# Kernel optimization log

Measured on AMD Instinct MI355X. Metric: run time of the kernel, lower is better.

Reference implementation:

```python
import jax, jax.numpy as jnp
import numpy as np

EMB = 1024
HEADS = 16
HEAD_DIM = EMB // HEADS
EPS = 1e-5


def layer_norm(x, scale, shift):
    mean = jnp.mean(x, axis=-1, keepdims=True)
    var = jnp.mean(jnp.square(x - mean), axis=-1, keepdims=True)  # unbiased=False
    return scale * ((x - mean) / jnp.sqrt(var + EPS)) + shift


def gelu_tanh(x):
    c = jnp.sqrt(jnp.asarray(2.0 / jnp.pi, x.dtype))
    return 0.5 * x * (1.0 + jnp.tanh(c * (x + 0.044715 * x * x * x)))


def setup_inputs() -> dict:
    key = jax.random.key(0)
    ks = jax.random.split(key, 12)
    s = 0.02
    B, S, D = 2, 2048, EMB
    return {
        "x": jax.random.normal(ks[0], (B, S, D), jnp.float32),
        "wq": jax.random.normal(ks[1], (D, D), jnp.float32) * s,
        "wk": jax.random.normal(ks[2], (D, D), jnp.float32) * s,
        "wv": jax.random.normal(ks[3], (D, D), jnp.float32) * s,
        "wo": jax.random.normal(ks[4], (D, D), jnp.float32) * s,
        "bo": jnp.zeros((D,), jnp.float32),
        "w1": jax.random.normal(ks[5], (D, 4 * D), jnp.float32) * s,
        "b1": jnp.zeros((4 * D,), jnp.float32),
        "w2": jax.random.normal(ks[6], (4 * D, D), jnp.float32) * s,
        "b2": jnp.zeros((D,), jnp.float32),
        "g1": jnp.ones((D,), jnp.float32),
        "s1": jnp.zeros((D,), jnp.float32),
        "g2": jnp.ones((D,), jnp.float32),
        "s2": jnp.zeros((D,), jnp.float32),
    }


def reference(x, wq, wk, wv, wo, bo, w1, b1, w2, b2, g1, s1, g2, s2):
    B, S, D = x.shape
    # --- attention sub-block ---
    h = layer_norm(x, g1, s1)
    q = (h @ wq).reshape(B, S, HEADS, HEAD_DIM).transpose(0, 2, 1, 3)  # [B,H,S,d]
    k = (h @ wk).reshape(B, S, HEADS, HEAD_DIM).transpose(0, 2, 1, 3)
    v = (h @ wv).reshape(B, S, HEADS, HEAD_DIM).transpose(0, 2, 1, 3)
    scores = jnp.einsum("bhqd,bhkd->bhqk", q, k)
    causal = jnp.tril(jnp.ones((S, S), bool))  # True = keep
    scores = jnp.where(causal, scores, -jnp.inf)
    attn = jax.nn.softmax(scores / jnp.sqrt(jnp.asarray(HEAD_DIM, x.dtype)), axis=-1)
    ctx = jnp.einsum("bhqk,bhkd->bhqd", attn, v).transpose(0, 2, 1, 3).reshape(B, S, D)
    x = x + (ctx @ wo + bo)
    # --- FFN sub-block ---
    h = layer_norm(x, g2, s2)
    h = gelu_tanh(h @ w1 + b1) @ w2 + b2
    return x + h
```

## Files before the change

kernel.cpp:

```cpp
#include <hip/hip_runtime.h>


typedef __attribute__((ext_vector_type(8))) short s16x8;
typedef __attribute__((ext_vector_type(4))) float f32x4;
typedef __attribute__((ext_vector_type(16))) float f32x16;
typedef unsigned short u16;
typedef unsigned int u32;

#define DEV static __device__ __forceinline__
#define MFMA16 __builtin_amdgcn_mfma_f32_16x16x32_bf16
#define MFMA32 __builtin_amdgcn_mfma_f32_32x32x16_bf16
#define GLOAD_LDS16(gp, lp)                                         \
  __builtin_amdgcn_global_load_lds(                                 \
      (const __attribute__((address_space(1))) void*)(gp),          \
      (__attribute__((address_space(3))) void*)(lp), 16, 0, 0)

DEV u16 f2bf(float f) {
  union { float f; unsigned u; } c; c.f = f;
  unsigned u = c.u;
  u += 0x7fff + ((u >> 16) & 1);
  return (u16)(u >> 16);
}

DEV u32 cvtpk(float lo, float hi) {
  u32 r;
  asm("v_cvt_pk_bf16_f32 %0, %1, %2" : "=v"(r) : "v"(lo), "v"(hi));
  return r;
}

DEV float gelu_tanh(float v) {
  const float c0 = 0.7978845608028654f;
  float u = c0 * (v + 0.044715f * v * v * v);
  return 0.5f * v * (1.0f + tanhf(u));
}

DEV s16x8 ld8(const u16* p) { return *(const s16x8*)p; }

__global__ __launch_bounds__(256) void tconv_kernel(
    const float* __restrict__ W, u16* __restrict__ Wt, int K, int N) {
  __shared__ u16 T[64][80];
  const int t = threadIdx.x;
  const int n0 = blockIdx.x * 64, k0 = blockIdx.y * 64;
  const int kr = t >> 4, nc = (t & 15) * 4;
#pragma unroll
  for (int p = 0; p < 4; ++p) {
    const int k = p * 16 + kr;
    float4 v = *(const float4*)(W + (size_t)(k0 + k) * N + n0 + nc);
    T[nc + 0][k] = f2bf(v.x);
    T[nc + 1][k] = f2bf(v.y);
    T[nc + 2][k] = f2bf(v.z);
    T[nc + 3][k] = f2bf(v.w);
  }
  __syncthreads();
  const int nr = t >> 2, kc = (t & 3) * 16;
  *(s16x8*)(Wt + (size_t)(n0 + nr) * K + k0 + kc) = *(const s16x8*)&T[nr][kc];
  *(s16x8*)(Wt + (size_t)(n0 + nr) * K + k0 + kc + 8) =
      *(const s16x8*)&T[nr][kc + 8];
}

__global__ __launch_bounds__(256) void ln_kernel(
    const float* __restrict__ x, const float* __restrict__ g,
    const float* __restrict__ b, u16* __restrict__ out) {
  const int row = blockIdx.x;
  const int t = threadIdx.x;
  const float* xr = x + (size_t)row * 1024;
  float4 v = *(const float4*)(xr + t * 4);
  float s = v.x + v.y + v.z + v.w;
  float ss = v.x * v.x + v.y * v.y + v.z * v.z + v.w * v.w;
#pragma unroll
  for (int off = 1; off < 64; off <<= 1) {
    s += __shfl_xor(s, off);
    ss += __shfl_xor(ss, off);
  }
  __shared__ float sb[4], ssb[4];
  const int w = t >> 6;
  if ((t & 63) == 0) { sb[w] = s; ssb[w] = ss; }
  __syncthreads();
  s = sb[0] + sb[1] + sb[2] + sb[3];
  ss = ssb[0] + ssb[1] + ssb[2] + ssb[3];
  const float mean = s * (1.0f / 1024.0f);
  const float var = ss * (1.0f / 1024.0f) - mean * mean;
  const float rstd = rsqrtf(var + 1e-5f);
  const int c = t * 4;
  ushort4 o;
  o.x = f2bf(g[c + 0] * ((v.x - mean) * rstd) + b[c + 0]);
  o.y = f2bf(g[c + 1] * ((v.y - mean) * rstd) + b[c + 1]);
  o.z = f2bf(g[c + 2] * ((v.z - mean) * rstd) + b[c + 2]);
  o.w = f2bf(g[c + 3] * ((v.w - mean) * rstd) + b[c + 3]);
  *(ushort4*)(out + (size_t)row * 1024 + c) = o;
}

DEV void gemm_stage(const u16* __restrict__ A, const u16* __restrict__ Bt,
                    int bm, int bn, int K, int kof, u16 (*Al)[32],
                    u16 (*Bl)[32], int w, int lane) {
  const int srow = lane >> 2;
  const int scol = ((lane & 3) ^ ((lane >> 3) & 3)) * 8;
#pragma unroll
  for (int p = 0; p < 2; ++p) {
    const int r0 = (w * 2 + p) * 16;
    GLOAD_LDS16(A + (size_t)(bm + r0 + srow) * K + kof + scol, &Al[r0][0]);
    GLOAD_LDS16(Bt + (size_t)(bn + r0 + srow) * K + kof + scol, &Bl[r0][0]);
  }
}

DEV void gemm_step(const u16 (*Al)[32], const u16 (*Bl)[32],
                   f32x4 (&acc)[4][4], int wm, int wn, int lr, int lg) {
  const int cs = (lg ^ ((lr >> 1) & 3)) * 8;
  s16x8 af[4], bf[4];
#pragma unroll
  for (int i = 0; i < 4; ++i) {
    af[i] = *(const s16x8*)&Al[wm + i * 16 + lr][cs];
    bf[i] = *(const s16x8*)&Bl[wn + i * 16 + lr][cs];
  }
#pragma unroll
  for (int i = 0; i < 4; ++i)
#pragma unroll
    for (int j = 0; j < 4; ++j)
      acc[i][j] = MFMA16(af[i], bf[j], acc[i][j], 0, 0, 0);
}

template <int EPI>
__global__ __launch_bounds__(256) void gemm_kernel(
    const u16* __restrict__ A, const u16* __restrict__ Bt,
    const float* __restrict__ bias, const float* __restrict__ res,
    void* __restrict__ Cv, int M, int N, int K) {
  __shared__ __align__(16) u16 Al[2][128][32];
  __shared__ __align__(16) u16 Bl[2][128][32];
  const int t = threadIdx.x;
  const int lane = t & 63, w = t >> 6;
  const int wm = (w >> 1) * 64, wn = (w & 1) * 64;
  int bid = blockIdx.y * gridDim.x + blockIdx.x;
  const int q8 = (gridDim.x * gridDim.y) >> 3;
  bid = (bid & 7) * q8 + (bid >> 3);
  const int bm = (bid / gridDim.x) * 128, bn = (bid % gridDim.x) * 128;
  const int lr = lane & 15, lg = lane >> 4;
  f32x4 acc[4][4] = {};
  const int nkt = K >> 5;

  gemm_stage(A, Bt, bm, bn, K, 0, Al[0], Bl[0], w, lane);
  __syncthreads();
  for (int kt = 0; kt < nkt - 1; ++kt) {
    const int cur = kt & 1;
    gemm_stage(A, Bt, bm, bn, K, (kt + 1) << 5, Al[cur ^ 1], Bl[cur ^ 1], w,
               lane);
    gemm_step(Al[cur], Bl[cur], acc, wm, wn, lr, lg);
    __syncthreads();
  }
  gemm_step(Al[(nkt - 1) & 1], Bl[(nkt - 1) & 1], acc, wm, wn, lr, lg);

#pragma unroll
  for (int i = 0; i < 4; ++i) {
    const int row = bm + wm + i * 16 + lg * 4;
#pragma unroll
    for (int j = 0; j < 4; ++j) {
      const int col = bn + wn + j * 16 + lr;
      if (EPI == 0) {
        const int bb = row >> 11, sloc = row & 2047;
        const int which = col >> 10, n = col & 1023;
        const int hh = n >> 6, dd = n & 63;
        u16* qbuf = (u16*)Cv;
        if (which == 2) {
          ushort4 o;
          o.x = f2bf(acc[i][j][0]); o.y = f2bf(acc[i][j][1]);
          o.z = f2bf(acc[i][j][2]); o.w = f2bf(acc[i][j][3]);
          *(ushort4*)(qbuf + 8388608 +
                      (size_t)((bb * 16 + hh) * 64 + dd) * 2048 + sloc) = o;
        } else {
          const float sc = (which == 0) ? 0.18033688011112042f : 1.0f;
          u16* dst = qbuf + (size_t)which * 4194304 +
                     ((size_t)(bb * 16 + hh) * 2048 + sloc) * 64 + dd;
#pragma unroll
          for (int e = 0; e < 4; ++e) dst[(size_t)e * 64] = f2bf(acc[i][j][e] * sc);
        }
      } else if (EPI == 1) {
        float* C = (float*)Cv;
        const float bs = bias[col];
#pragma unroll
        for (int e = 0; e < 4; ++e)
          C[(size_t)(row + e) * N + col] =
              acc[i][j][e] + bs + res[(size_t)(row + e) * N + col];
      } else {
        u16* C = (u16*)Cv;
        const float bs = bias[col];
#pragma unroll
        for (int e = 0; e < 4; ++e)
          C[(size_t)(row + e) * N + col] = f2bf(gelu_tanh(acc[i][j][e] + bs));
      }
    }
  }
}

DEV void g64_stage(const u16* __restrict__ A, const u16* __restrict__ Bt,
                   int bm, int bn, int K, int kof, u16 (*Al)[32],
                   u16 (*Bl)[32], int w, int lane) {
  const int srow = lane >> 2;
  const int scol = ((lane & 3) ^ ((lane >> 3) & 3)) * 8;
  const int r0 = w << 4;
  GLOAD_LDS16(A + (size_t)(bm + r0 + srow) * K + kof + scol, &Al[r0][0]);
  GLOAD_LDS16(Bt + (size_t)(bn + r0 + srow) * K + kof + scol, &Bl[r0][0]);
}

DEV void g64_step(const u16 (*Al)[32], const u16 (*Bl)[32],
                  f32x4 (&acc)[2][2], int wm, int wn, int lr, int lg) {
  const int cs = (lg ^ ((lr >> 1) & 3)) * 8;
  s16x8 af[2], bf[2];
#pragma unroll
  for (int i = 0; i < 2; ++i) {
    af[i] = *(const s16x8*)&Al[wm + i * 16 + lr][cs];
    bf[i] = *(const s16x8*)&Bl[wn + i * 16 + lr][cs];
  }
#pragma unroll
  for (int i = 0; i < 2; ++i)
#pragma unroll
    for (int j = 0; j < 2; ++j)
      acc[i][j] = MFMA16(af[i], bf[j], acc[i][j], 0, 0, 0);
}

template <int EPI>
__global__ __launch_bounds__(256) void gemm64_kernel(
    const u16* __restrict__ A, const u16* __restrict__ Bt,
    const float* __restrict__ bias, const float* __restrict__ res,
    void* __restrict__ Cv, int M, int N, int K) {
  __shared__ __align__(16) u16 Al[2][64][32];
  __shared__ __align__(16) u16 Bl[2][64][32];
  const int t = threadIdx.x;
  const int lane = t & 63, w = t >> 6;
  const int wm = (w >> 1) * 32, wn = (w & 1) * 32;
  int bid = blockIdx.y * gridDim.x + blockIdx.x;
  const int q8 = (gridDim.x * gridDim.y) >> 3;
  bid = (bid & 7) * q8 + (bid >> 3);
  const int bm = (bid / gridDim.x) * 64, bn = (bid % gridDim.x) * 64;
  const int lr = lane & 15, lg = lane >> 4;
  f32x4 acc[2][2] = {};
  const int nkt = K >> 5;

  g64_stage(A, Bt, bm, bn, K, 0, Al[0], Bl[0], w, lane);
  __syncthreads();
  for (int kt = 0; kt < nkt - 1; ++kt) {
    const int cur = kt & 1;
    g64_stage(A, Bt, bm, bn, K, (kt + 1) << 5, Al[cur ^ 1], Bl[cur ^ 1], w,
              lane);
    g64_step(Al[cur], Bl[cur], acc, wm, wn, lr, lg);
    __syncthreads();
  }
  g64_step(Al[(nkt - 1) & 1], Bl[(nkt - 1) & 1], acc, wm, wn, lr, lg);

#pragma unroll
  for (int i = 0; i < 2; ++i) {
    const int row = bm + wm + i * 16 + lg * 4;
#pragma unroll
    for (int j = 0; j < 2; ++j) {
      const int col = bn + wn + j * 16 + lr;
      if (EPI == 1) {
        float* C = (float*)Cv;
        const float bs = bias[col];
#pragma unroll
        for (int e = 0; e < 4; ++e)
          C[(size_t)(row + e) * N + col] =
              acc[i][j][e] + bs + res[(size_t)(row + e) * N + col];
      } else {
        u16* C = (u16*)Cv;
        const float bs = bias[col];
#pragma unroll
        for (int e = 0; e < 4; ++e)
          C[(size_t)(row + e) * N + col] = f2bf(gelu_tanh(acc[i][j][e] + bs));
      }
    }
  }
}

DEV void g256_stage(const u16* __restrict__ A, const u16* __restrict__ Bt,
                    int bm, int bn, int K, int kof, u16 (*Al)[32],
                    u16 (*Bl)[32], int w, int lane) {
  const int srow = lane >> 2;
  const int scol = ((lane & 3) ^ ((lane >> 3) & 3)) * 8;
#pragma unroll
  for (int c = 0; c < 2; ++c) {
    const int r0 = (w << 5) + (c << 4);
    GLOAD_LDS16(A + (size_t)(bm + r0 + srow) * K + kof + scol, &Al[r0][0]);
    GLOAD_LDS16(Bt + (size_t)(bn + r0 + srow) * K + kof + scol, &Bl[r0][0]);
  }
}

DEV void g256_step(const u16 (*Al)[32], const u16 (*Bl)[32],
                   f32x4 (&acc)[8][4], int wm, int wn, int lr, int lg) {
  const int cs = (lg ^ ((lr >> 1) & 3)) * 8;
  s16x8 af[8], bf[4];
#pragma unroll
  for (int i = 0; i < 8; ++i)
    af[i] = *(const s16x8*)&Al[wm + i * 16 + lr][cs];
#pragma unroll
  for (int j = 0; j < 4; ++j)
    bf[j] = *(const s16x8*)&Bl[wn + j * 16 + lr][cs];
#pragma unroll
  for (int i = 0; i < 8; ++i)
#pragma unroll
    for (int j = 0; j < 4; ++j)
      acc[i][j] = MFMA16(af[i], bf[j], acc[i][j], 0, 0, 0);
}

template <int EPI>
__global__ __launch_bounds__(512, 2) void gemm256_kernel(
    const u16* __restrict__ A, const u16* __restrict__ Bt,
    const float* __restrict__ bias, const float* __restrict__ res,
    void* __restrict__ Cv, int M, int N, int K) {
  __shared__ __align__(16) u16 Al[2][256][32];
  __shared__ __align__(16) u16 Bl[2][256][32];
  const int t = threadIdx.x;
  const int lane = t & 63, w = t >> 6;
  const int wm = (w >> 2) << 7;
  const int wn = (w & 3) << 6;
  int bid = blockIdx.y * gridDim.x + blockIdx.x;
  const int q8 = (gridDim.x * gridDim.y) >> 3;
  bid = (bid & 7) * q8 + (bid >> 3);
  const int bm = (bid / gridDim.x) << 8, bn = (bid % gridDim.x) << 8;
  const int lr = lane & 15, lg = lane >> 4;
  f32x4 acc[8][4] = {};
  const int nkt = K >> 5;

  g256_stage(A, Bt, bm, bn, K, 0, Al[0], Bl[0], w, lane);
  __syncthreads();
  for (int kt = 0; kt < nkt - 1; ++kt) {
    const int cur = kt & 1;
    g256_stage(A, Bt, bm, bn, K, (kt + 1) << 5, Al[cur ^ 1], Bl[cur ^ 1], w,
               lane);
    g256_step(Al[cur], Bl[cur], acc, wm, wn, lr, lg);
    __syncthreads();
  }
  g256_step(Al[(nkt - 1) & 1], Bl[(nkt - 1) & 1], acc, wm, wn, lr, lg);

#pragma unroll
  for (int i = 0; i < 8; ++i) {
    const int row = bm + wm + i * 16 + lg * 4;
#pragma unroll
    for (int j = 0; j < 4; ++j) {
      const int col = bn + wn + j * 16 + lr;
      if (EPI == 1) {
        float* C = (float*)Cv;
        const float bs = bias[col];
#pragma unroll
        for (int e = 0; e < 4; ++e)
          C[(size_t)(row + e) * N + col] =
              acc[i][j][e] + bs + res[(size_t)(row + e) * N + col];
      } else {
        u16* C = (u16*)Cv;
        const float bs = bias[col];
#pragma unroll
        for (int e = 0; e < 4; ++e)
          C[(size_t)(row + e) * N + col] = f2bf(gelu_tanh(acc[i][j][e] + bs));
      }
    }
  }
}

DEV float vmax16(const f32x16& v) {
  float a = fmaxf(v[0], v[1]), b = fmaxf(v[2], v[3]);
  float c = fmaxf(v[4], v[5]), d = fmaxf(v[6], v[7]);
  float e = fmaxf(v[8], v[9]), f = fmaxf(v[10], v[11]);
  float g = fmaxf(v[12], v[13]), h = fmaxf(v[14], v[15]);
  a = fmaxf(a, b); c = fmaxf(c, d); e = fmaxf(e, f); g = fmaxf(g, h);
  return fmaxf(fmaxf(a, c), fmaxf(e, g));
}
DEV float vsum16(const f32x16& v) {
  float a = v[0] + v[1], b = v[2] + v[3];
  float c = v[4] + v[5], d = v[6] + v[7];
  float e = v[8] + v[9], f = v[10] + v[11];
  float g = v[12] + v[13], h = v[14] + v[15];
  a += b; c += d; e += f; g += h;
  return (a + c) + (e + g);
}

struct A32 {
  s16x8 q[4];
  f32x16 o0, o1;
  float m, l;
};

template <int MODE>
DEV void body32(A32& st, int k0, const u16* Kb, const u16* Vb, int la,
                int hi) {
  s16x8 ka0[4], ka1[4];
#pragma unroll
  for (int c = 0; c < 4; ++c)
    ka0[c] = ld8(Kb + (size_t)(k0 + la) * 64 + c * 16 + hi * 8);
  if (MODE != 2)
#pragma unroll
    for (int c = 0; c < 4; ++c)
      ka1[c] = ld8(Kb + (size_t)(k0 + 32 + la) * 64 + c * 16 + hi * 8);
  f32x16 s0, s1;
#pragma unroll
  for (int r = 0; r < 16; ++r) { s0[r] = 0.f; s1[r] = 0.f; }
#pragma unroll
  for (int c = 0; c < 4; ++c) s0 = MFMA32(ka0[c], st.q[c], s0, 0, 0, 0);
  if (MODE != 2)
#pragma unroll
    for (int c = 0; c < 4; ++c) s1 = MFMA32(ka1[c], st.q[c], s1, 0, 0, 0);
  const int nkc = (MODE == 2) ? 2 : 4;
  s16x8 va0[4], va1[4];
#pragma unroll
  for (int kc = 0; kc < 4; ++kc)
    if (kc < nkc) {
      va0[kc] = ld8(Vb + (size_t)la * 2048 + k0 + kc * 16 + hi * 8);
      va1[kc] = ld8(Vb + (size_t)(32 + la) * 2048 + k0 + kc * 16 + hi * 8);
    }
  if (MODE == 1) {
#pragma unroll
    for (int r = 0; r < 16; ++r) {
      const int kl = (r & 3) + 8 * (r >> 2) + 4 * hi;
      if (kl > la) s1[r] = -INFINITY;
    }
  }
  if (MODE == 2) {
#pragma unroll
    for (int r = 0; r < 16; ++r) {
      const int kl = (r & 3) + 8 * (r >> 2) + 4 * hi;
      if (kl > la) s0[r] = -INFINITY;
    }
  }
  float mt = vmax16(s0);
  if (MODE != 2) mt = fmaxf(mt, vmax16(s1));
  mt = fmaxf(mt, __shfl_xor(mt, 32));
  const float mn = fmaxf(st.m, mt);
  const float sf = exp2f(st.m - mn);
#pragma unroll
  for (int r = 0; r < 16; ++r) s0[r] = exp2f(s0[r] - mn);
  if (MODE != 2)
#pragma unroll
    for (int r = 0; r < 16; ++r) s1[r] = exp2f(s1[r] - mn);
  float rs = vsum16(s0);
  if (MODE != 2) rs += vsum16(s1);
  rs += __shfl_xor(rs, 32);
  st.l = st.l * sf + rs;
  st.m = mn;
#pragma unroll
  for (int r = 0; r < 16; ++r) { st.o0[r] *= sf; st.o1[r] *= sf; }
  const int nh = (MODE == 2) ? 1 : 2;
#pragma unroll
  for (int half = 0; half < nh; ++half) {
    u32 w[8];
#pragma unroll
    for (int i = 0; i < 8; ++i)
      w[i] = half ? cvtpk(s1[2 * i], s1[2 * i + 1])
                  : cvtpk(s0[2 * i], s0[2 * i + 1]);
#pragma unroll
    for (int kp = 0; kp < 2; ++kp) {
      const u32 w0 = w[4 * kp + 0], w1 = w[4 * kp + 1];
      const u32 w2 = w[4 * kp + 2], w3 = w[4 * kp + 3];
      const u32 t0 = hi ? w0 : w2, t1 = hi ? w1 : w3;
      const u32 x0 = (u32)__shfl_xor((int)t0, 32);
      const u32 x1 = (u32)__shfl_xor((int)t1, 32);
      union { u32 u[4]; s16x8 v; } bb;
      bb.u[0] = hi ? x0 : w0;
      bb.u[1] = hi ? x1 : w1;
      bb.u[2] = hi ? w2 : x0;
      bb.u[3] = hi ? w3 : x1;
      const int kc = half * 2 + kp;
      st.o0 = MFMA32(va0[kc], bb.v, st.o0, 0, 0, 0);
      st.o1 = MFMA32(va1[kc], bb.v, st.o1, 0, 0, 0);
    }
  }
}

DEV void a32_init(A32& st, const u16* Qbase, int qs, int la, int hi) {
#pragma unroll
  for (int c = 0; c < 4; ++c)
    st.q[c] = ld8(Qbase + (size_t)(qs + la) * 64 + c * 16 + hi * 8);
#pragma unroll
  for (int r = 0; r < 16; ++r) { st.o0[r] = 0.f; st.o1[r] = 0.f; }
  st.m = -INFINITY;
  st.l = 0.f;
}

DEV void a32_fin(const A32& st, u16* __restrict__ ctx, int bh, int qs, int la,
                 int hi) {
  const int bb = bh >> 4, hh = bh & 15;
  const float inv = 1.0f / st.l;
  u16* crow = ctx + (size_t)(bb * 2048 + qs + la) * 1024 + hh * 64;
#pragma unroll
  for (int r = 0; r < 16; r += 2) {
    const int d = (r & 3) + 8 * (r >> 2) + 4 * hi;
    *(u32*)(crow + d) = cvtpk(st.o0[r] * inv, st.o0[r + 1] * inv);
    *(u32*)(crow + 32 + d) = cvtpk(st.o1[r] * inv, st.o1[r + 1] * inv);
  }
}

template <bool ODD>
DEV void chain_tail(A32& st, int nfull, int qs, const u16* Kb, const u16* Vb,
                    int la, int hi) {
  if (ODD) body32<1>(st, nfull * 64, Kb, Vb, la, hi);
  else     body32<2>(st, qs, Kb, Vb, la, hi);
}

__global__ __launch_bounds__(64) void attn_kernel(
    const u16* __restrict__ Qg, const u16* __restrict__ Kg,
    const u16* __restrict__ Vt, u16* __restrict__ ctx) {
  const int lane = threadIdx.x & 63;
  const int la = lane & 31, hi = lane >> 5;
  const int tA = blockIdx.x;
  const int bh = blockIdx.y;
  const int tB = 63 - tA;
  const int qsA = tA * 32, qsB = tB * 32;
  const int nfA = tA >> 1, nfB = tB >> 1;
  const size_t baseK = (size_t)bh * 2048 * 64;
  const size_t baseV = (size_t)bh * 64 * 2048;
  const u16* Kb = Kg + baseK;
  const u16* Vb = Vt + baseV;

  A32 A, B;
  a32_init(A, Qg + baseK, qsA, la, hi);
  a32_init(B, Qg + baseK, qsB, la, hi);

  for (int kt = 0; kt < nfA; ++kt) {
    body32<0>(B, kt * 64, Kb, Vb, la, hi);
    body32<0>(A, kt * 64, Kb, Vb, la, hi);
  }
  body32<0>(B, nfA * 64, Kb, Vb, la, hi);
  if (tA & 1) chain_tail<true>(A, nfA, qsA, Kb, Vb, la, hi);
  else        chain_tail<false>(A, nfA, qsA, Kb, Vb, la, hi);
  a32_fin(A, ctx, bh, qsA, la, hi);

  for (int kt = nfA + 1; kt < nfB; ++kt)
    body32<0>(B, kt * 64, Kb, Vb, la, hi);
  if (tB & 1) chain_tail<true>(B, nfB, qsB, Kb, Vb, la, hi);
  else        chain_tail<false>(B, nfB, qsB, Kb, Vb, la, hi);
  a32_fin(B, ctx, bh, qsB, la, hi);
}

extern "C" void kernel_launch(void* const* d_in, const int* in_sizes, int n_in,
                              void* d_out, int out_size, void* d_ws,
                              size_t ws_size, hipStream_t stream) {
  const float* x  = (const float*)d_in[0];
  const float* wq = (const float*)d_in[1];
  const float* wk = (const float*)d_in[2];
  const float* wv = (const float*)d_in[3];
  const float* wo = (const float*)d_in[4];
  const float* bo = (const float*)d_in[5];
  const float* w1 = (const float*)d_in[6];
  const float* b1 = (const float*)d_in[7];
  const float* w2 = (const float*)d_in[8];
  const float* b2 = (const float*)d_in[9];
  const float* g1 = (const float*)d_in[10];
  const float* s1 = (const float*)d_in[11];
  const float* g2 = (const float*)d_in[12];
  const float* s2 = (const float*)d_in[13];
  float* out = (float*)d_out;

  const size_t MB = (size_t)1 << 20;
  char* p = (char*)d_ws;
  u16* hb    = (u16*)(p + 0 * MB);
  u16* qbuf  = (u16*)(p + 8 * MB);
  u16* ctxb  = (u16*)(p + 32 * MB);
  float* x2  = (float*)(p + 40 * MB);
  u16* h2b   = (u16*)(p + 56 * MB);
  u16* qkvw  = (u16*)(p + 64 * MB);
  u16* wot   = (u16*)(p + 70 * MB);
  u16* w1t   = (u16*)(p + 72 * MB);
  u16* w2t   = (u16*)(p + 80 * MB);
  u16* gb    = (u16*)(p + 0 * MB);

  const dim3 blk(256);
  tconv_kernel<<<dim3(16, 16), blk, 0, stream>>>(wq, qkvw, 1024, 1024);
  tconv_kernel<<<dim3(16, 16), blk, 0, stream>>>(wk, qkvw + 1048576, 1024, 1024);
  tconv_kernel<<<dim3(16, 16), blk, 0, stream>>>(wv, qkvw + 2097152, 1024, 1024);
  tconv_kernel<<<dim3(16, 16), blk, 0, stream>>>(wo, wot, 1024, 1024);
  tconv_kernel<<<dim3(64, 16), blk, 0, stream>>>(w1, w1t, 1024, 4096);
  tconv_kernel<<<dim3(16, 64), blk, 0, stream>>>(w2, w2t, 4096, 1024);

  ln_kernel<<<4096, blk, 0, stream>>>(x, g1, s1, hb);
  gemm_kernel<0><<<dim3(24, 32), blk, 0, stream>>>(hb, qkvw, nullptr, nullptr,
                                                   qbuf, 4096, 3072, 1024);
  attn_kernel<<<dim3(32, 32), dim3(64), 0, stream>>>(
      qbuf, qbuf + 4194304, qbuf + 8388608, ctxb);
  gemm64_kernel<1><<<dim3(16, 64), blk, 0, stream>>>(ctxb, wot, bo, x, x2,
                                                     4096, 1024, 1024);
  ln_kernel<<<4096, blk, 0, stream>>>(x2, g2, s2, h2b);
  gemm256_kernel<2><<<dim3(16, 16), dim3(512), 0, stream>>>(
      h2b, w1t, b1, nullptr, gb, 4096, 4096, 1024);
  gemm64_kernel<1><<<dim3(16, 64), blk, 0, stream>>>(gb, w2t, b2, x2, out,
                                                     4096, 1024, 4096);
}
```

Measured before the change: 302.5 us.

## Split attention KV range across two blocks with combine pass, merge weight conversions

Result: no change. 301.6 us (-0.3%).

```diff
diff --git a/kernel.cpp b/kernel.cpp
--- a/kernel.cpp
+++ b/kernel.cpp
@@ -22,6 +22,11 @@
   return (u16)(u >> 16);
 }
 
+DEV float bf2f(u16 v) {
+  union { u32 u; float f; } c; c.u = (u32)v << 16;
+  return c.f;
+}
+
 DEV u32 cvtpk(float lo, float hi) {
   u32 r;
   asm("v_cvt_pk_bf16_f32 %0, %1, %2" : "=v"(r) : "v"(lo), "v"(hi));
@@ -36,11 +41,10 @@
 
 DEV s16x8 ld8(const u16* p) { return *(const s16x8*)p; }
 
-__global__ __launch_bounds__(256) void tconv_kernel(
-    const float* __restrict__ W, u16* __restrict__ Wt, int K, int N) {
+DEV void tconv_tile(const float* __restrict__ W, u16* __restrict__ Wt, int K,
+                    int N, int bx, int by, int t) {
   __shared__ u16 T[64][80];
-  const int t = threadIdx.x;
-  const int n0 = blockIdx.x * 64, k0 = blockIdx.y * 64;
+  const int n0 = bx * 64, k0 = by * 64;
   const int kr = t >> 4, nc = (t & 15) * 4;
 #pragma unroll
   for (int p = 0; p < 4; ++p) {
@@ -56,6 +60,29 @@
   *(s16x8*)(Wt + (size_t)(n0 + nr) * K + k0 + kc) = *(const s16x8*)&T[nr][kc];
   *(s16x8*)(Wt + (size_t)(n0 + nr) * K + k0 + kc + 8) =
       *(const s16x8*)&T[nr][kc + 8];
+}
+
+__global__ __launch_bounds__(256) void tconv_all(
+    const float* __restrict__ wq, const float* __restrict__ wk,
+    const float* __restrict__ wv, const float* __restrict__ wo,
+    const float* __restrict__ w1, const float* __restrict__ w2,
+    u16* __restrict__ qkvw, u16* __restrict__ wot, u16* __restrict__ w1t,
+    u16* __restrict__ w2t) {
+  const int idx = blockIdx.x, t = threadIdx.x;
+  if (idx < 768) {
+    const int which = idx >> 8, r = idx & 255;
+    const float* W = which == 0 ? wq : (which == 1 ? wk : wv);
+    tconv_tile(W, qkvw + which * 1048576, 1024, 1024, r & 15, r >> 4, t);
+  } else if (idx < 1024) {
+    const int r = idx - 768;
+    tconv_tile(wo, wot, 1024, 1024, r & 15, r >> 4, t);
+  } else if (idx < 2048) {
+    const int r = idx - 1024;
+    tconv_tile(w1, w1t, 1024, 4096, r & 63, r >> 6, t);
+  } else {
+    const int r = idx - 2048;
+    tconv_tile(w2, w2t, 4096, 1024, r & 15, r >> 4, t);
+  }
 }
 
 __global__ __launch_bounds__(256) void ln_kernel(
@@ -420,8 +447,9 @@
   float mt = vmax16(s0);
   if (MODE != 2) mt = fmaxf(mt, vmax16(s1));
   mt = fmaxf(mt, __shfl_xor(mt, 32));
-  const float mn = fmaxf(st.m, mt);
-  const float sf = exp2f(st.m - mn);
+  const bool skip = __all(mt <= st.m + 8.0f) != 0;
+  const float mn = skip ? st.m : fmaxf(st.m, mt);
+  const float sf = skip ? 1.0f : exp2f(st.m - mn);
 #pragma unroll
   for (int r = 0; r < 16; ++r) s0[r] = exp2f(s0[r] - mn);
   if (MODE != 2)
@@ -430,10 +458,12 @@
   float rs = vsum16(s0);
   if (MODE != 2) rs += vsum16(s1);
   rs += __shfl_xor(rs, 32);
-  st.l = st.l * sf + rs;
+  st.l = skip ? (st.l + rs) : (st.l * sf + rs);
   st.m = mn;
-#pragma unroll
-  for (int r = 0; r < 16; ++r) { st.o0[r] *= sf; st.o1[r] *= sf; }
+  if (!skip) {
+#pragma unroll
+    for (int r = 0; r < 16; ++r) { st.o0[r] *= sf; st.o1[r] *= sf; }
+  }
   const int nh = (MODE == 2) ? 1 : 2;
 #pragma unroll
   for (int half = 0; half < nh; ++half) {
@@ -471,36 +501,45 @@
   st.l = 0.f;
 }
 
-DEV void a32_fin(const A32& st, u16* __restrict__ ctx, int bh, int qs, int la,
-                 int hi) {
-  const int bb = bh >> 4, hh = bh & 15;
-  const float inv = 1.0f / st.l;
-  u16* crow = ctx + (size_t)(bb * 2048 + qs + la) * 1024 + hh * 64;
+DEV void a32_emit(const A32& st, u16* __restrict__ pO, float* __restrict__ pml,
+                  int p, int la, int hi) {
+  u16* po = pO + (size_t)p * 2048 + la * 64;
 #pragma unroll
   for (int r = 0; r < 16; r += 2) {
     const int d = (r & 3) + 8 * (r >> 2) + 4 * hi;
-    *(u32*)(crow + d) = cvtpk(st.o0[r] * inv, st.o0[r + 1] * inv);
-    *(u32*)(crow + 32 + d) = cvtpk(st.o1[r] * inv, st.o1[r + 1] * inv);
-  }
-}
-
-template <bool ODD>
-DEV void chain_tail(A32& st, int nfull, int qs, const u16* Kb, const u16* Vb,
-                    int la, int hi) {
-  if (ODD) body32<1>(st, nfull * 64, Kb, Vb, la, hi);
-  else     body32<2>(st, qs, Kb, Vb, la, hi);
+    *(u32*)(po + d) = cvtpk(st.o0[r], st.o0[r + 1]);
+    *(u32*)(po + 32 + d) = cvtpk(st.o1[r], st.o1[r + 1]);
+  }
+  if (hi == 0) {
+    pml[p * 64 + la] = st.m;
+    pml[p * 64 + 32 + la] = st.l;
+  }
+}
+
+DEV void body_tail(A32& st, int t, const u16* Kb, const u16* Vb, int la,
+                   int hi) {
+  const int nf = t >> 1;
+  if (t & 1) body32<1>(st, nf * 64, Kb, Vb, la, hi);
+  else       body32<2>(st, nf * 64, Kb, Vb, la, hi);
 }
 
 __global__ __launch_bounds__(64) void attn_kernel(
     const u16* __restrict__ Qg, const u16* __restrict__ Kg,
-    const u16* __restrict__ Vt, u16* __restrict__ ctx) {
+    const u16* __restrict__ Vt, u16* __restrict__ pO,
+    float* __restrict__ pml) {
   const int lane = threadIdx.x & 63;
   const int la = lane & 31, hi = lane >> 5;
-  const int tA = blockIdx.x;
+  const int tA = blockIdx.x >> 1, h = blockIdx.x & 1;
   const int bh = blockIdx.y;
   const int tB = 63 - tA;
   const int qsA = tA * 32, qsB = tB * 32;
-  const int nfA = tA >> 1, nfB = tB >> 1;
+  const int nA = (tA >> 1) + 1, nB = (tB >> 1) + 1;
+  const int cA = (nA + 1) >> 1, cB = (nB + 1) >> 1;
+  const int a0 = h ? cA : 0, a1 = h ? nA : cA;
+  const int b0 = h ? cB : 0, b1 = h ? nB : cB;
+  const int aiEnd = min(a1, nA - 1), biEnd = min(b1, nB - 1);
+  const bool aTail = (a1 == nA) && (a1 > a0);
+  const bool bTail = (b1 == nB) && (b1 > b0);
   const size_t baseK = (size_t)bh * 2048 * 64;
   const size_t baseV = (size_t)bh * 64 * 2048;
   const u16* Kb = Kg + baseK;
@@ -510,20 +549,54 @@
   a32_init(A, Qg + baseK, qsA, la, hi);
   a32_init(B, Qg + baseK, qsB, la, hi);
 
-  for (int kt = 0; kt < nfA; ++kt) {
-    body32<0>(B, kt * 64, Kb, Vb, la, hi);
-    body32<0>(A, kt * 64, Kb, Vb, la, hi);
-  }
-  body32<0>(B, nfA * 64, Kb, Vb, la, hi);
-  if (tA & 1) chain_tail<true>(A, nfA, qsA, Kb, Vb, la, hi);
-  else        chain_tail<false>(A, nfA, qsA, Kb, Vb, la, hi);
-  a32_fin(A, ctx, bh, qsA, la, hi);
-
-  for (int kt = nfA + 1; kt < nfB; ++kt)
-    body32<0>(B, kt * 64, Kb, Vb, la, hi);
-  if (tB & 1) chain_tail<true>(B, nfB, qsB, Kb, Vb, la, hi);
-  else        chain_tail<false>(B, nfB, qsB, Kb, Vb, la, hi);
-  a32_fin(B, ctx, bh, qsB, la, hi);
+  int ia = a0, ib = b0;
+  const int common = min(aiEnd - a0, biEnd - b0);
+  for (int i = 0; i < common; ++i) {
+    body32<0>(B, ib * 64, Kb, Vb, la, hi); ++ib;
+    body32<0>(A, ia * 64, Kb, Vb, la, hi); ++ia;
+  }
+  for (; ib < biEnd; ++ib) body32<0>(B, ib * 64, Kb, Vb, la, hi);
+  for (; ia < aiEnd; ++ia) body32<0>(A, ia * 64, Kb, Vb, la, hi);
+  if (bTail) body_tail(B, tB, Kb, Vb, la, hi);
+  if (aTail) body_tail(A, tA, Kb, Vb, la, hi);
+
+  const int pA = (((bh << 6) | tA) << 1) | h;
+  const int pB = (((bh << 6) | tB) << 1) | h;
+  a32_emit(A, pO, pml, pA, la, hi);
+  a32_emit(B, pO, pml, pB, la, hi);
+}
+
+__global__ __launch_bounds__(64) void attn_combine(
+    const u16* __restrict__ pO, const float* __restrict__ pml,
+    u16* __restrict__ ctx) {
+  const int t = blockIdx.x, bh = blockIdx.y;
+  const int lane = threadIdx.x & 63;
+  const int la = lane & 31, hi = lane >> 5;
+  const int p0 = ((bh << 6) | t) << 1;
+  const float m0 = pml[p0 * 64 + la], l0 = pml[p0 * 64 + 32 + la];
+  const float m1 = pml[(p0 + 1) * 64 + la], l1 = pml[(p0 + 1) * 64 + 32 + la];
+  const float M = fmaxf(m0, m1);
+  const float w0 = exp2f(m0 - M), w1 = exp2f(m1 - M);
+  const float inv = 1.0f / (l0 * w0 + l1 * w1);
+  const float f0 = w0 * inv, f1 = w1 * inv;
+  const u16* o0 = pO + (size_t)p0 * 2048 + la * 64 + hi * 32;
+  const u16* o1 = o0 + 2048;
+  const int bb = bh >> 4, hh = bh & 15;
+  u16* crow = ctx + (size_t)(bb * 2048 + t * 32 + la) * 1024 + hh * 64 +
+              hi * 32;
+#pragma unroll
+  for (int j = 0; j < 32; j += 8) {
+    s16x8 a = ld8(o0 + j), b = ld8(o1 + j);
+    union { u32 u[4]; s16x8 v; } o;
+#pragma unroll
+    for (int i = 0; i < 4; ++i) {
+      const float e0 = bf2f((u16)a[2 * i]) * f0 + bf2f((u16)b[2 * i]) * f1;
+      const float e1 =
+          bf2f((u16)a[2 * i + 1]) * f0 + bf2f((u16)b[2 * i + 1]) * f1;
+      o.u[i] = cvtpk(e0, e1);
+    }
+    *(s16x8*)(crow + j) = o.v;
+  }
 }
 
 extern "C" void kernel_launch(void* const* d_in, const int* in_sizes, int n_in,
@@ -550,27 +623,25 @@
   u16* hb    = (u16*)(p + 0 * MB);
   u16* qbuf  = (u16*)(p + 8 * MB);
   u16* ctxb  = (u16*)(p + 32 * MB);
+  u16* pO    = (u16*)(p + 40 * MB);
   float* x2  = (float*)(p + 40 * MB);
-  u16* h2b   = (u16*)(p + 56 * MB);
-  u16* qkvw  = (u16*)(p + 64 * MB);
-  u16* wot   = (u16*)(p + 70 * MB);
-  u16* w1t   = (u16*)(p + 72 * MB);
-  u16* w2t   = (u16*)(p + 80 * MB);
+  float* pml = (float*)(p + 56 * MB);
+  u16* h2b   = (u16*)(p + 57 * MB);
+  u16* qkvw  = (u16*)(p + 65 * MB);
+  u16* wot   = (u16*)(p + 71 * MB);
+  u16* w1t   = (u16*)(p + 73 * MB);
+  u16* w2t   = (u16*)(p + 81 * MB);
   u16* gb    = (u16*)(p + 0 * MB);
 
   const dim3 blk(256);
-  tconv_kernel<<<dim3(16, 16), blk, 0, stream>>>(wq, qkvw, 1024, 1024);
-  tconv_kernel<<<dim3(16, 16), blk, 0, stream>>>(wk, qkvw + 1048576, 1024, 1024);
-  tconv_kernel<<<dim3(16, 16), blk, 0, stream>>>(wv, qkvw + 2097152, 1024, 1024);
-  tconv_kernel<<<dim3(16, 16), blk, 0, stream>>>(wo, wot, 1024, 1024);
-  tconv_kernel<<<dim3(64, 16), blk, 0, stream>>>(w1, w1t, 1024, 4096);
-  tconv_kernel<<<dim3(16, 64), blk, 0, stream>>>(w2, w2t, 4096, 1024);
-
+  tconv_all<<<dim3(3072), blk, 0, stream>>>(wq, wk, wv, wo, w1, w2, qkvw, wot,
+                                            w1t, w2t);
   ln_kernel<<<4096, blk, 0, stream>>>(x, g1, s1, hb);
   gemm_kernel<0><<<dim3(24, 32), blk, 0, stream>>>(hb, qkvw, nullptr, nullptr,
                                                    qbuf, 4096, 3072, 1024);
-  attn_kernel<<<dim3(32, 32), dim3(64), 0, stream>>>(
-      qbuf, qbuf + 4194304, qbuf + 8388608, ctxb);
+  attn_kernel<<<dim3(64, 32), dim3(64), 0, stream>>>(
+      qbuf, qbuf + 4194304, qbuf + 8388608, pO, pml);
+  attn_combine<<<dim3(64, 32), dim3(64), 0, stream>>>(pO, pml, ctxb);
   gemm64_kernel<1><<<dim3(16, 64), blk, 0, stream>>>(ctxb, wot, bo, x, x2,
                                                      4096, 1024, 1024);
   ln_kernel<<<4096, blk, 0, stream>>>(x2, g2, s2, h2b);
```
